# Kernel optimization log

Measured on AMD Instinct MI355X. Metric: run time of the kernel, lower is better.

Reference implementation:

```python
import jax, jax.numpy as jnp
import numpy as np

DEPTH = 10
NUM_FEATURES = 512
NUM_LEAVES = 2 ** DEPTH
TEMPERATURE = 0.1
BATCH = 32768


def _leaf_codes():
    # codes[leaf, i] = bit i (MSB first) of leaf index
    leaves = np.arange(NUM_LEAVES)
    shifts = DEPTH - 1 - np.arange(DEPTH)
    codes = (leaves[:, None] >> shifts[None, :]) & 1
    return jnp.asarray(codes, dtype=jnp.float32)  # [num_leaves, depth]


def setup_inputs() -> dict:
    key = jax.random.key(0)
    k1, k2, k3 = jax.random.split(key, 3)
    x = jax.random.normal(k1, (BATCH, NUM_FEATURES), dtype=jnp.float32)
    feature_weights = jax.random.normal(k2, (DEPTH, NUM_FEATURES), dtype=jnp.float32) * 0.01
    thresholds = jnp.zeros((DEPTH,), dtype=jnp.float32)
    leaf_values = jax.random.normal(k3, (NUM_FEATURES, NUM_LEAVES), dtype=jnp.float32) * 0.01
    return {"x": x, "feature_weights": feature_weights,
            "thresholds": thresholds, "leaf_values": leaf_values}


def reference(x, feature_weights, thresholds, leaf_values):
    codes = _leaf_codes()                                   # [L, D]
    probs = jax.nn.softmax(feature_weights, axis=1)          # [D, F]
    sel = x @ probs.T                                        # [B, D]
    decisions = jax.nn.sigmoid((sel - thresholds) / TEMPERATURE)  # [B, D]
    # leaf_probs[b, l] = prod_d (p*code + (1-p)*(1-code))
    p = decisions[:, None, :]                                # [B, 1, D]
    c = codes[None, :, :]                                    # [1, L, D]
    leaf_probs = jnp.prod(p * c + (1.0 - p) * (1.0 - c), axis=-1)  # [B, L]
    out = leaf_probs @ leaf_values.T                         # [B, F]
    return out
```

## Files before the change

### kernel.cpp

```cpp
#include <hip/hip_runtime.h>
#include <hip/hip_bf16.h>
#include <cstdint>

using u16 = unsigned short;
using u32 = unsigned int;

#define DEPTH 10
#define NF 512
#define NL 1024
#define BATCH_N 32768
#define TEMP_INV 10.0f
#define GBM 128
#define GBN 256
#define GBK 64
#define NSTEP (NL / GBK)

typedef float f32x4 __attribute__((ext_vector_type(4)));
typedef short s16x8 __attribute__((ext_vector_type(8)));
typedef __bf16 bf16x8 __attribute__((ext_vector_type(8)));

__device__ __forceinline__ u16 f2bf(float f) {
  u32 u = __float_as_uint(f);
  u = (u + 0x7fffu + ((u >> 16) & 1u)) >> 16;
  return (u16)u;
}

__device__ __forceinline__ void gld_lds16(const void* g, void* lds) {
  __builtin_amdgcn_global_load_lds(
      (const __attribute__((address_space(1))) void*)g,
      (__attribute__((address_space(3))) void*)lds, 16, 0, 0);
}

__global__ void k_cvt(const float* __restrict__ lv, u16* __restrict__ lvb) {
  int i = (blockIdx.x * blockDim.x + threadIdx.x) * 8;
  float4 a = *(const float4*)(lv + i);
  float4 b = *(const float4*)(lv + i + 4);
  uint4 u;
  u.x = f2bf(a.x) | ((u32)f2bf(a.y) << 16);
  u.y = f2bf(a.z) | ((u32)f2bf(a.w) << 16);
  u.z = f2bf(b.x) | ((u32)f2bf(b.y) << 16);
  u.w = f2bf(b.z) | ((u32)f2bf(b.w) << 16);
  *(uint4*)(lvb + i) = u;
}

__global__ __launch_bounds__(256, 4) void k_sel(const float* __restrict__ x,
                                                const float* __restrict__ fw,
                                                const float* __restrict__ thr,
                                                float* __restrict__ pout) {
  __shared__ float Ps[DEPTH * NF];
  const int tid = threadIdx.x;
  const int lane = tid & 63;
  const int w = tid >> 6;

  for (int d = w; d < DEPTH; d += 4) {
    const float* row = fw + d * NF;
    float v[8];
    float mx = -1e30f;
#pragma unroll
    for (int i = 0; i < 8; ++i) { v[i] = row[lane * 8 + i]; mx = fmaxf(mx, v[i]); }
#pragma unroll
    for (int s = 32; s >= 1; s >>= 1) mx = fmaxf(mx, __shfl_xor(mx, s));
    float sum = 0.f;
#pragma unroll
    for (int i = 0; i < 8; ++i) { v[i] = __expf(v[i] - mx); sum += v[i]; }
#pragma unroll
    for (int s = 32; s >= 1; s >>= 1) sum += __shfl_xor(sum, s);
    float inv = 1.0f / sum;
#pragma unroll
    for (int i = 0; i < 8; ++i) Ps[d * NF + lane * 8 + i] = v[i] * inv;
  }
  __syncthreads();

  const int g = lane & 15;
  const int qr = lane >> 4;
  const int r0 = blockIdx.x * 32 + (w * 4 + qr) * 2;
  const float* xp0 = x + (size_t)r0 * NF + g * 4;
  const float* xp1 = xp0 + NF;

  float a0[DEPTH], a1[DEPTH];
#pragma unroll
  for (int d = 0; d < DEPTH; ++d) { a0[d] = 0.f; a1[d] = 0.f; }
#pragma unroll 2
  for (int i = 0; i < 8; ++i) {
    float4 xv0 = *(const float4*)(xp0 + i * 64);
    float4 xv1 = *(const float4*)(xp1 + i * 64);
    const float* pb = &Ps[i * 64 + g * 4];
#pragma unroll
    for (int d = 0; d < DEPTH; ++d) {
      f32x4 pv = *(const f32x4*)(pb + d * NF);
      a0[d] += xv0.x * pv[0] + xv0.y * pv[1] + xv0.z * pv[2] + xv0.w * pv[3];
      a1[d] += xv1.x * pv[0] + xv1.y * pv[1] + xv1.z * pv[2] + xv1.w * pv[3];
    }
  }
#pragma unroll
  for (int d = 0; d < DEPTH; ++d) {
    a0[d] += __shfl_xor(a0[d], 1); a0[d] += __shfl_xor(a0[d], 2);
    a0[d] += __shfl_xor(a0[d], 4); a0[d] += __shfl_xor(a0[d], 8);
    a1[d] += __shfl_xor(a1[d], 1); a1[d] += __shfl_xor(a1[d], 2);
    a1[d] += __shfl_xor(a1[d], 4); a1[d] += __shfl_xor(a1[d], 8);
  }
  if (g < DEPTH) {
    float s0 = (g == 0) ? a0[0] : (g == 1) ? a0[1] : (g == 2) ? a0[2]
             : (g == 3) ? a0[3] : (g == 4) ? a0[4] : (g == 5) ? a0[5]
             : (g == 6) ? a0[6] : (g == 7) ? a0[7] : (g == 8) ? a0[8] : a0[9];
    float s1 = (g == 0) ? a1[0] : (g == 1) ? a1[1] : (g == 2) ? a1[2]
             : (g == 3) ? a1[3] : (g == 4) ? a1[4] : (g == 5) ? a1[5]
             : (g == 6) ? a1[6] : (g == 7) ? a1[7] : (g == 8) ? a1[8] : a1[9];
    float t = thr[g];
    pout[(size_t)r0 * DEPTH + g]       = 1.0f / (1.0f + __expf(-(s0 - t) * TEMP_INV));
    pout[(size_t)(r0 + 1) * DEPTH + g] = 1.0f / (1.0f + __expf(-(s1 - t) * TEMP_INV));
  }
}

__global__ __launch_bounds__(256, 2) void k_gemm(const u16* __restrict__ B,
                                                 const float* __restrict__ p,
                                                 float* __restrict__ C) {
  __shared__ char smem[65536];
  const int tid = threadIdx.x;
  const int lane = tid & 63;
  const int w = tid >> 6;
  const int wm = w >> 1, wn = w & 1;
  const int bm = blockIdx.x >> 1, bn = blockIdx.x & 1;
  const int brow = bm * GBM, bcol = bn * GBN;
  const int rA = lane & 15, sg = lane >> 4;

  float T[4][8];
  float base0[4], r0_[4], r1_[4], r2_[4], r3_[4], r4_[4];
#pragma unroll
  for (int m = 0; m < 4; ++m) {
    const float* pr = p + (size_t)(brow + wm * 64 + m * 16 + rA) * DEPTH;
    float p0 = pr[0], p1 = pr[1], p2 = pr[2], p3 = pr[3], p4 = pr[4];
    float p5 = pr[5], p6 = pr[6], p7 = pr[7], p8 = pr[8], p9 = pr[9];
    float q0 = 1.f - p0, q1 = 1.f - p1, q2 = 1.f - p2, q3 = 1.f - p3, q4 = 1.f - p4;
    base0[m] = q0 * q1 * q2 * q3 * q4;
    r0_[m] = p0 / q0; r1_[m] = p1 / q1; r2_[m] = p2 / q2;
    r3_[m] = p3 / q3; r4_[m] = p4 / q4;
    float s56 = ((sg & 2) ? p5 : 1.f - p5) * ((sg & 1) ? p6 : 1.f - p6);
    float a7 = 1.f - p7, b7 = p7, a8 = 1.f - p8, b8 = p8, a9 = 1.f - p9, b9 = p9;
#pragma unroll
    for (int j = 0; j < 8; ++j)
      T[m][j] = s56 * ((j & 4) ? b7 : a7) * ((j & 2) ? b8 : a8) * ((j & 1) ? b9 : a9);
  }

  f32x4 acc[4][8];
#pragma unroll
  for (int m = 0; m < 4; ++m)
#pragma unroll
    for (int n = 0; n < 8; ++n) acc[m][n] = {0.f, 0.f, 0.f, 0.f};

  auto STAGE = [&](int step, int buf) {
    char* bsb = smem + buf * 32768;
#pragma unroll
    for (int it = 0; it < 8; ++it) {
      int lin = it * 256 + tid;
      int r = lin >> 3;
      int sl = (lin & 7) ^ (r & 7);
      gld_lds16(B + (size_t)(bcol + r) * NL + step * GBK + sl * 8, bsb + lin * 16);
    }
  };

  STAGE(0, 0);
  asm volatile("s_waitcnt vmcnt(0)" ::: "memory");
  __builtin_amdgcn_s_barrier();

#pragma unroll 1
  for (int kk = 0; kk < NSTEP; ++kk) {
    if (kk < NSTEP - 1) STAGE(kk + 1, (kk + 1) & 1);
    const char* bb = smem + (kk & 1) * 32768;

    float H[4];
#pragma unroll
    for (int m = 0; m < 4; ++m) {
      float g = base0[m] * ((kk & 8) ? r0_[m] : 1.0f);
      g *= (kk & 4) ? r1_[m] : 1.0f;
      g *= (kk & 2) ? r2_[m] : 1.0f;
      g *= (kk & 1) ? r3_[m] : 1.0f;
      H[m] = g;
    }
    {
      bf16x8 af[4];
#pragma unroll
      for (int m = 0; m < 4; ++m)
#pragma unroll
        for (int j = 0; j < 8; ++j) af[m][j] = (__bf16)(H[m] * T[m][j]);
#pragma unroll
      for (int n = 0; n < 8; ++n) {
        int row = wn * 128 + n * 16 + rA;
        bf16x8 bf = __builtin_bit_cast(bf16x8,
            *(const s16x8*)(bb + row * 128 + ((sg ^ (row & 7)) << 4)));
        acc[0][n] = __builtin_amdgcn_mfma_f32_16x16x32_bf16(af[0], bf, acc[0][n], 0, 0, 0);
        acc[1][n] = __builtin_amdgcn_mfma_f32_16x16x32_bf16(af[1], bf, acc[1][n], 0, 0, 0);
        acc[2][n] = __builtin_amdgcn_mfma_f32_16x16x32_bf16(af[2], bf, acc[2][n], 0, 0, 0);
        acc[3][n] = __builtin_amdgcn_mfma_f32_16x16x32_bf16(af[3], bf, acc[3][n], 0, 0, 0);
      }
    }
    {
      bf16x8 af[4];
#pragma unroll
      for (int m = 0; m < 4; ++m) {
        float h1 = H[m] * r4_[m];
#pragma unroll
        for (int j = 0; j < 8; ++j) af[m][j] = (__bf16)(h1 * T[m][j]);
      }
#pragma unroll
      for (int n = 0; n < 8; ++n) {
        int row = wn * 128 + n * 16 + rA;
        bf16x8 bf = __builtin_bit_cast(bf16x8,
            *(const s16x8*)(bb + row * 128 + (((4 + sg) ^ (row & 7)) << 4)));
        acc[0][n] = __builtin_amdgcn_mfma_f32_16x16x32_bf16(af[0], bf, acc[0][n], 0, 0, 0);
        acc[1][n] = __builtin_amdgcn_mfma_f32_16x16x32_bf16(af[1], bf, acc[1][n], 0, 0, 0);
        acc[2][n] = __builtin_amdgcn_mfma_f32_16x16x32_bf16(af[2], bf, acc[2][n], 0, 0, 0);
        acc[3][n] = __builtin_amdgcn_mfma_f32_16x16x32_bf16(af[3], bf, acc[3][n], 0, 0, 0);
      }
    }
    if (kk < NSTEP - 1) {
      asm volatile("s_waitcnt vmcnt(0) lgkmcnt(0)" ::: "memory");
      __builtin_amdgcn_s_barrier();
    }
  }

  const int c0 = lane & 15;
  const int rr = (lane >> 4) * 4;
#pragma unroll
  for (int m = 0; m < 4; ++m)
#pragma unroll
    for (int n = 0; n < 8; ++n) {
      int col = bcol + wn * 128 + n * 16 + c0;
#pragma unroll
      for (int r = 0; r < 4; ++r)
        C[(size_t)(brow + wm * 64 + m * 16 + rr + r) * NF + col] = acc[m][n][r];
    }
}

extern "C" void kernel_launch(void* const* d_in, const int* in_sizes, int n_in,
                              void* d_out, int out_size, void* d_ws, size_t ws_size,
                              hipStream_t stream) {
  const float* x  = (const float*)d_in[0];
  const float* fw = (const float*)d_in[1];
  const float* th = (const float*)d_in[2];
  const float* lv = (const float*)d_in[3];
  float* out = (float*)d_out;

  u16* lvb = (u16*)d_ws;
  float* pbuf = (float*)((char*)d_ws + NF * NL * 2);

  k_cvt<<<(NF * NL / 8) / 256, 256, 0, stream>>>(lv, lvb);
  k_sel<<<BATCH_N / 32, 256, 0, stream>>>(x, fw, th, pbuf);
  k_gemm<<<(BATCH_N / GBM) * 2, 256, 0, stream>>>(lvb, pbuf, out);
}
```

Before: 67.23 us.

## Restructure GEMM into 8-wave blocks with triple-buffered half-K LDS pipeline

Raises the GEMM block from 4 to 8 waves, so each wave owns 32 rows instead of 64 and holds half the accumulators. B tiles are split into 128-column by 64-K halves in a 6-slot LDS ring. Loads are issued two steps ahead in small chunks interleaved with four MFMA phases per K step, and s_setprio is raised around the MFMA bursts. The goal is to overlap global-to-LDS traffic with matrix work and raise per-CU wave parallelism. In exchange it uses 96KB of LDS per block and many more barriers, which may limit residency to one block per CU.

```diff
diff --git a/kernel.cpp b/kernel.cpp
--- a/kernel.cpp
+++ b/kernel.cpp
@@ -13,7 +13,7 @@
 #define GBM 128
 #define GBN 256
 #define GBK 64
-#define NSTEP (NL / GBK)
+#define NSTEP 16
 
 typedef float f32x4 __attribute__((ext_vector_type(4)));
 typedef short s16x8 __attribute__((ext_vector_type(8)));
@@ -112,29 +112,28 @@
   }
 }
 
-__global__ __launch_bounds__(256, 2) void k_gemm(const u16* __restrict__ B,
+__global__ __launch_bounds__(512, 2) void k_gemm(const u16* __restrict__ B,
                                                  const float* __restrict__ p,
                                                  float* __restrict__ C) {
-  __shared__ char smem[65536];
+  __shared__ char smem[98304];
   const int tid = threadIdx.x;
   const int lane = tid & 63;
   const int w = tid >> 6;
-  const int wm = w >> 1, wn = w & 1;
-  const int bm = blockIdx.x >> 1, bn = blockIdx.x & 1;
+  const int wm = w >> 1;
+  const int wn = w & 1;
+  const int bm = (int)blockIdx.x >> 1, bn = (int)blockIdx.x & 1;
   const int brow = bm * GBM, bcol = bn * GBN;
   const int rA = lane & 15, sg = lane >> 4;
 
-  float T[4][8];
-  float base0[4], r0_[4], r1_[4], r2_[4], r3_[4], r4_[4];
-#pragma unroll
-  for (int m = 0; m < 4; ++m) {
-    const float* pr = p + (size_t)(brow + wm * 64 + m * 16 + rA) * DEPTH;
+  float T[2][8], base0[2], R0[2], R1[2], R2[2], R3[2], R4[2];
+#pragma unroll
+  for (int m = 0; m < 2; ++m) {
+    const float* pr = p + (size_t)(brow + wm * 32 + m * 16 + rA) * DEPTH;
     float p0 = pr[0], p1 = pr[1], p2 = pr[2], p3 = pr[3], p4 = pr[4];
     float p5 = pr[5], p6 = pr[6], p7 = pr[7], p8 = pr[8], p9 = pr[9];
     float q0 = 1.f - p0, q1 = 1.f - p1, q2 = 1.f - p2, q3 = 1.f - p3, q4 = 1.f - p4;
     base0[m] = q0 * q1 * q2 * q3 * q4;
-    r0_[m] = p0 / q0; r1_[m] = p1 / q1; r2_[m] = p2 / q2;
-    r3_[m] = p3 / q3; r4_[m] = p4 / q4;
+    R0[m] = p0 / q0; R1[m] = p1 / q1; R2[m] = p2 / q2; R3[m] = p3 / q3; R4[m] = p4 / q4;
     float s56 = ((sg & 2) ? p5 : 1.f - p5) * ((sg & 1) ? p6 : 1.f - p6);
     float a7 = 1.f - p7, b7 = p7, a8 = 1.f - p8, b8 = p8, a9 = 1.f - p9, b9 = p9;
 #pragma unroll
@@ -142,93 +141,108 @@
       T[m][j] = s56 * ((j & 4) ? b7 : a7) * ((j & 2) ? b8 : a8) * ((j & 1) ? b9 : a9);
   }
 
-  f32x4 acc[4][8];
-#pragma unroll
-  for (int m = 0; m < 4; ++m)
+  f32x4 acc[2][8];
+#pragma unroll
+  for (int m = 0; m < 2; ++m)
 #pragma unroll
     for (int n = 0; n < 8; ++n) acc[m][n] = {0.f, 0.f, 0.f, 0.f};
 
-  auto STAGE = [&](int step, int buf) {
-    char* bsb = smem + buf * 32768;
-#pragma unroll
-    for (int it = 0; it < 8; ++it) {
-      int lin = it * 256 + tid;
-      int r = lin >> 3;
-      int sl = (lin & 7) ^ (r & 7);
-      gld_lds16(B + (size_t)(bcol + r) * NL + step * GBK + sl * 8, bsb + lin * 16);
-    }
+  auto STAGE1 = [&](int h, int buf, int it) {
+    int lin = it * 512 + tid;
+    int r = lin >> 3, s = lin & 7;
+    gld_lds16(B + (size_t)(bcol + (h & 1) * 128 + r) * NL + (h >> 1) * GBK + ((s ^ (r & 7)) * 8),
+              smem + buf * 16384 + lin * 16);
   };
 
-  STAGE(0, 0);
-  asm volatile("s_waitcnt vmcnt(0)" ::: "memory");
+#pragma unroll
+  for (int h = 0; h < 4; ++h) { STAGE1(h, h, 0); STAGE1(h, h, 1); }
+  asm volatile("s_waitcnt vmcnt(4)" ::: "memory");
   __builtin_amdgcn_s_barrier();
+
+  int b0 = 0;
+  bf16x8 af0, af1;
+  float Ha, Hb;
+
+#define DO_PHASE(KH, NH, SIDX, TRAILBAR)                                        \
+  {                                                                             \
+    const char* bb = smem + (b0 + wn) * 16384;                                  \
+    int rr0 = ((NH) * 4 + 0) * 16 + rA;                                         \
+    int rr1 = ((NH) * 4 + 1) * 16 + rA;                                         \
+    int rr2 = ((NH) * 4 + 2) * 16 + rA;                                         \
+    int rr3 = ((NH) * 4 + 3) * 16 + rA;                                         \
+    bf16x8 f0 = __builtin_bit_cast(bf16x8,                                      \
+        *(const s16x8*)(bb + rr0 * 128 + ((((KH)*4 + sg) ^ (rr0 & 7)) << 4)));  \
+    bf16x8 f1 = __builtin_bit_cast(bf16x8,                                      \
+        *(const s16x8*)(bb + rr1 * 128 + ((((KH)*4 + sg) ^ (rr1 & 7)) << 4)));  \
+    bf16x8 f2 = __builtin_bit_cast(bf16x8,                                      \
+        *(const s16x8*)(bb + rr2 * 128 + ((((KH)*4 + sg) ^ (rr2 & 7)) << 4)));  \
+    bf16x8 f3 = __builtin_bit_cast(bf16x8,                                      \
+        *(const s16x8*)(bb + rr3 * 128 + ((((KH)*4 + sg) ^ (rr3 & 7)) << 4)));  \
+    if ((SIDX) == 0) {                         \
+      Ha = base0[0] * ((kk & 8) ? R0[0] : 1.f);                                 \
+      Ha *= (kk & 4) ? R1[0] : 1.f;  Ha *= (kk & 2) ? R2[0] : 1.f;              \
+      Ha *= (kk & 1) ? R3[0] : 1.f;                                             \
+      Hb = base0[1] * ((kk & 8) ? R0[1] : 1.f);                                 \
+      Hb *= (kk & 4) ? R1[1] : 1.f;  Hb *= (kk & 2) ? R2[1] : 1.f;              \
+      Hb *= (kk & 1) ? R3[1] : 1.f;                                             \
+      _Pragma("unroll") for (int j = 0; j < 8; ++j) {                           \
+        af0[j] = (__bf16)(Ha * T[0][j]);  af1[j] = (__bf16)(Hb * T[1][j]);      \
+      }                                                                         \
+    }                                                                           \
+    if ((SIDX) == 2) {                                 \
+      Ha *= R4[0];  Hb *= R4[1];                                                \
+      _Pragma("unroll") for (int j = 0; j < 8; ++j) {                           \
+        af0[j] = (__bf16)(Ha * T[0][j]);  af1[j] = (__bf16)(Hb * T[1][j]);      \
+      }                                                                         \
+    }                                                                           \
+    if (kk < NSTEP - 2) {                        \
+      int sb = b0 + 4 + ((SIDX) >> 1); if (sb >= 6) sb -= 6;                    \
+      STAGE1(2 * kk + 4 + ((SIDX) >> 1), sb, (SIDX) & 1);                       \
+    }                                                                           \
+    __builtin_amdgcn_s_barrier();                                               \
+    asm volatile("s_waitcnt lgkmcnt(0)" ::: "memory");                          \
+    __builtin_amdgcn_sched_barrier(0);                                          \
+    __builtin_amdgcn_s_setprio(1);                                              \
+    acc[0][(NH)*4+0] = __builtin_amdgcn_mfma_f32_16x16x32_bf16(af0, f0, acc[0][(NH)*4+0], 0, 0, 0); \
+    acc[1][(NH)*4+0] = __builtin_amdgcn_mfma_f32_16x16x32_bf16(af1, f0, acc[1][(NH)*4+0], 0, 0, 0); \
+    acc[0][(NH)*4+1] = __builtin_amdgcn_mfma_f32_16x16x32_bf16(af0, f1, acc[0][(NH)*4+1], 0, 0, 0); \
+    acc[1][(NH)*4+1] = __builtin_amdgcn_mfma_f32_16x16x32_bf16(af1, f1, acc[1][(NH)*4+1], 0, 0, 0); \
+    acc[0][(NH)*4+2] = __builtin_amdgcn_mfma_f32_16x16x32_bf16(af0, f2, acc[0][(NH)*4+2], 0, 0, 0); \
+    acc[1][(NH)*4+2] = __builtin_amdgcn_mfma_f32_16x16x32_bf16(af1, f2, acc[1][(NH)*4+2], 0, 0, 0); \
+    acc[0][(NH)*4+3] = __builtin_amdgcn_mfma_f32_16x16x32_bf16(af0, f3, acc[0][(NH)*4+3], 0, 0, 0); \
+    acc[1][(NH)*4+3] = __builtin_amdgcn_mfma_f32_16x16x32_bf16(af1, f3, acc[1][(NH)*4+3], 0, 0, 0); \
+    __builtin_amdgcn_s_setprio(0);                                              \
+    if (TRAILBAR) __builtin_amdgcn_s_barrier();                                 \
+  }
 
 #pragma unroll 1
   for (int kk = 0; kk < NSTEP; ++kk) {
-    if (kk < NSTEP - 1) STAGE(kk + 1, (kk + 1) & 1);
-    const char* bb = smem + (kk & 1) * 32768;
-
-    float H[4];
-#pragma unroll
-    for (int m = 0; m < 4; ++m) {
-      float g = base0[m] * ((kk & 8) ? r0_[m] : 1.0f);
-      g *= (kk & 4) ? r1_[m] : 1.0f;
-      g *= (kk & 2) ? r2_[m] : 1.0f;
-      g *= (kk & 1) ? r3_[m] : 1.0f;
-      H[m] = g;
+    DO_PHASE(0, 0, 0, 1)
+    DO_PHASE(0, 1, 1, 1)
+    DO_PHASE(1, 0, 2, 1)
+    DO_PHASE(1, 1, 3, 0)
+    if (kk < NSTEP - 1) {
+      if (kk == NSTEP - 2) {
+        asm volatile("s_waitcnt vmcnt(0)" ::: "memory");
+      } else {
+        asm volatile("s_waitcnt vmcnt(4)" ::: "memory");
+      }
+      __builtin_amdgcn_s_barrier();
+      b0 += 2; if (b0 >= 6) b0 -= 6;
     }
-    {
-      bf16x8 af[4];
-#pragma unroll
-      for (int m = 0; m < 4; ++m)
-#pragma unroll
-        for (int j = 0; j < 8; ++j) af[m][j] = (__bf16)(H[m] * T[m][j]);
-#pragma unroll
-      for (int n = 0; n < 8; ++n) {
-        int row = wn * 128 + n * 16 + rA;
-        bf16x8 bf = __builtin_bit_cast(bf16x8,
-            *(const s16x8*)(bb + row * 128 + ((sg ^ (row & 7)) << 4)));
-        acc[0][n] = __builtin_amdgcn_mfma_f32_16x16x32_bf16(af[0], bf, acc[0][n], 0, 0, 0);
-        acc[1][n] = __builtin_amdgcn_mfma_f32_16x16x32_bf16(af[1], bf, acc[1][n], 0, 0, 0);
-        acc[2][n] = __builtin_amdgcn_mfma_f32_16x16x32_bf16(af[2], bf, acc[2][n], 0, 0, 0);
-        acc[3][n] = __builtin_amdgcn_mfma_f32_16x16x32_bf16(af[3], bf, acc[3][n], 0, 0, 0);
-      }
-    }
-    {
-      bf16x8 af[4];
-#pragma unroll
-      for (int m = 0; m < 4; ++m) {
-        float h1 = H[m] * r4_[m];
-#pragma unroll
-        for (int j = 0; j < 8; ++j) af[m][j] = (__bf16)(h1 * T[m][j]);
-      }
-#pragma unroll
-      for (int n = 0; n < 8; ++n) {
-        int row = wn * 128 + n * 16 + rA;
-        bf16x8 bf = __builtin_bit_cast(bf16x8,
-            *(const s16x8*)(bb + row * 128 + (((4 + sg) ^ (row & 7)) << 4)));
-        acc[0][n] = __builtin_amdgcn_mfma_f32_16x16x32_bf16(af[0], bf, acc[0][n], 0, 0, 0);
-        acc[1][n] = __builtin_amdgcn_mfma_f32_16x16x32_bf16(af[1], bf, acc[1][n], 0, 0, 0);
-        acc[2][n] = __builtin_amdgcn_mfma_f32_16x16x32_bf16(af[2], bf, acc[2][n], 0, 0, 0);
-        acc[3][n] = __builtin_amdgcn_mfma_f32_16x16x32_bf16(af[3], bf, acc[3][n], 0, 0, 0);
-      }
-    }
-    if (kk < NSTEP - 1) {
-      asm volatile("s_waitcnt vmcnt(0) lgkmcnt(0)" ::: "memory");
-      __builtin_amdgcn_s_barrier();
-    }
-  }
+  }
+#undef DO_PHASE
 
   const int c0 = lane & 15;
   const int rr = (lane >> 4) * 4;
 #pragma unroll
-  for (int m = 0; m < 4; ++m)
+  for (int m = 0; m < 2; ++m)
 #pragma unroll
     for (int n = 0; n < 8; ++n) {
       int col = bcol + wn * 128 + n * 16 + c0;
 #pragma unroll
       for (int r = 0; r < 4; ++r)
-        C[(size_t)(brow + wm * 64 + m * 16 + rr + r) * NF + col] = acc[m][n][r];
+        C[(size_t)(brow + wm * 32 + m * 16 + rr + r) * NF + col] = acc[m][n][r];
     }
 }
 
@@ -246,5 +260,5 @@
 
   k_cvt<<<(NF * NL / 8) / 256, 256, 0, stream>>>(lv, lvb);
   k_sel<<<BATCH_N / 32, 256, 0, stream>>>(x, fw, th, pbuf);
-  k_gemm<<<(BATCH_N / GBM) * 2, 256, 0, stream>>>(lvb, pbuf, out);
-}
+  k_gemm<<<(BATCH_N / GBM) * 2, 512, 0, stream>>>(lvb, pbuf, out);
+}
```

New measurement: 76.16 us. +13.3%, slower.

## Use 512-thread GEMM blocks and register-staged LDS loads instead of direct global-to-LDS

Applied to the files above, without the earlier changes.

The GEMM block grows from 4 to 8 waves, so each wave now owns 32 rows instead of 64, halving its accumulator registers and raising the occupancy target. The direct global_load_lds staging is replaced with ordinary global loads into registers, written to the swizzled LDS buffer after the MFMAs, with __syncthreads in place of hand-written waitcnt and barrier. The aim is better latency hiding through more resident waves. In exchange each B fragment read from LDS now feeds only two MFMAs instead of four, and the staging adds VGPR traffic and an extra LDS write pass.

```diff
diff --git a/kernel.cpp b/kernel.cpp
--- a/kernel.cpp
+++ b/kernel.cpp
@@ -13,7 +13,7 @@
 #define GBM 128
 #define GBN 256
 #define GBK 64
-#define NSTEP (NL / GBK)
+#define NSTEP 16
 
 typedef float f32x4 __attribute__((ext_vector_type(4)));
 typedef short s16x8 __attribute__((ext_vector_type(8)));
@@ -23,12 +23,6 @@
   u32 u = __float_as_uint(f);
   u = (u + 0x7fffu + ((u >> 16) & 1u)) >> 16;
   return (u16)u;
-}
-
-__device__ __forceinline__ void gld_lds16(const void* g, void* lds) {
-  __builtin_amdgcn_global_load_lds(
-      (const __attribute__((address_space(1))) void*)g,
-      (__attribute__((address_space(3))) void*)lds, 16, 0, 0);
 }
 
 __global__ void k_cvt(const float* __restrict__ lv, u16* __restrict__ lvb) {
@@ -112,29 +106,28 @@
   }
 }
 
-__global__ __launch_bounds__(256, 2) void k_gemm(const u16* __restrict__ B,
+__global__ __launch_bounds__(512, 4) void k_gemm(const u16* __restrict__ B,
                                                  const float* __restrict__ p,
                                                  float* __restrict__ C) {
   __shared__ char smem[65536];
   const int tid = threadIdx.x;
   const int lane = tid & 63;
   const int w = tid >> 6;
-  const int wm = w >> 1, wn = w & 1;
-  const int bm = blockIdx.x >> 1, bn = blockIdx.x & 1;
+  const int wm = w >> 1;
+  const int wn = w & 1;
+  const int bm = (int)blockIdx.x >> 1, bn = (int)blockIdx.x & 1;
   const int brow = bm * GBM, bcol = bn * GBN;
   const int rA = lane & 15, sg = lane >> 4;
 
-  float T[4][8];
-  float base0[4], r0_[4], r1_[4], r2_[4], r3_[4], r4_[4];
-#pragma unroll
-  for (int m = 0; m < 4; ++m) {
-    const float* pr = p + (size_t)(brow + wm * 64 + m * 16 + rA) * DEPTH;
+  float T[2][8], base0[2], R0[2], R1[2], R2[2], R3[2], R4[2];
+#pragma unroll
+  for (int m = 0; m < 2; ++m) {
+    const float* pr = p + (size_t)(brow + wm * 32 + m * 16 + rA) * DEPTH;
     float p0 = pr[0], p1 = pr[1], p2 = pr[2], p3 = pr[3], p4 = pr[4];
     float p5 = pr[5], p6 = pr[6], p7 = pr[7], p8 = pr[8], p9 = pr[9];
     float q0 = 1.f - p0, q1 = 1.f - p1, q2 = 1.f - p2, q3 = 1.f - p3, q4 = 1.f - p4;
     base0[m] = q0 * q1 * q2 * q3 * q4;
-    r0_[m] = p0 / q0; r1_[m] = p1 / q1; r2_[m] = p2 / q2;
-    r3_[m] = p3 / q3; r4_[m] = p4 / q4;
+    R0[m] = p0 / q0; R1[m] = p1 / q1; R2[m] = p2 / q2; R3[m] = p3 / q3; R4[m] = p4 / q4;
     float s56 = ((sg & 2) ? p5 : 1.f - p5) * ((sg & 1) ? p6 : 1.f - p6);
     float a7 = 1.f - p7, b7 = p7, a8 = 1.f - p8, b8 = p8, a9 = 1.f - p9, b9 = p9;
 #pragma unroll
@@ -142,93 +135,82 @@
       T[m][j] = s56 * ((j & 4) ? b7 : a7) * ((j & 2) ? b8 : a8) * ((j & 1) ? b9 : a9);
   }
 
-  f32x4 acc[4][8];
-#pragma unroll
-  for (int m = 0; m < 4; ++m)
+  f32x4 acc[2][8];
+#pragma unroll
+  for (int m = 0; m < 2; ++m)
 #pragma unroll
     for (int n = 0; n < 8; ++n) acc[m][n] = {0.f, 0.f, 0.f, 0.f};
 
-  auto STAGE = [&](int step, int buf) {
-    char* bsb = smem + buf * 32768;
-#pragma unroll
-    for (int it = 0; it < 8; ++it) {
-      int lin = it * 256 + tid;
-      int r = lin >> 3;
-      int sl = (lin & 7) ^ (r & 7);
-      gld_lds16(B + (size_t)(bcol + r) * NL + step * GBK + sl * 8, bsb + lin * 16);
+  const int sr = tid >> 3;
+  const int ss = tid & 7;
+  const int swz = (ss ^ (sr & 7)) * 16;
+
+  uint4 stg[4];
+  auto STAGE_LOAD = [&](int step) {
+#pragma unroll
+    for (int it = 0; it < 4; ++it) {
+      int r = it * 64 + sr;
+      stg[it] = *(const uint4*)(B + (size_t)(bcol + r) * NL + step * GBK + ss * 8);
     }
   };
-
-  STAGE(0, 0);
-  asm volatile("s_waitcnt vmcnt(0)" ::: "memory");
-  __builtin_amdgcn_s_barrier();
+  auto STAGE_WRITE = [&](int buf) {
+#pragma unroll
+    for (int it = 0; it < 4; ++it) {
+      int r = it * 64 + sr;
+      *(uint4*)(smem + buf * 32768 + r * 128 + swz) = stg[it];
+    }
+  };
+
+  STAGE_LOAD(0);
+  STAGE_WRITE(0);
+  __syncthreads();
 
 #pragma unroll 1
   for (int kk = 0; kk < NSTEP; ++kk) {
-    if (kk < NSTEP - 1) STAGE(kk + 1, (kk + 1) & 1);
+    if (kk < NSTEP - 1) STAGE_LOAD(kk + 1);
     const char* bb = smem + (kk & 1) * 32768;
 
-    float H[4];
-#pragma unroll
-    for (int m = 0; m < 4; ++m) {
-      float g = base0[m] * ((kk & 8) ? r0_[m] : 1.0f);
-      g *= (kk & 4) ? r1_[m] : 1.0f;
-      g *= (kk & 2) ? r2_[m] : 1.0f;
-      g *= (kk & 1) ? r3_[m] : 1.0f;
-      H[m] = g;
-    }
-    {
-      bf16x8 af[4];
-#pragma unroll
-      for (int m = 0; m < 4; ++m)
-#pragma unroll
-        for (int j = 0; j < 8; ++j) af[m][j] = (__bf16)(H[m] * T[m][j]);
+    float Ha = base0[0] * ((kk & 8) ? R0[0] : 1.f);
+    Ha *= (kk & 4) ? R1[0] : 1.f;
+    Ha *= (kk & 2) ? R2[0] : 1.f;
+    Ha *= (kk & 1) ? R3[0] : 1.f;
+    float Hb = base0[1] * ((kk & 8) ? R0[1] : 1.f);
+    Hb *= (kk & 4) ? R1[1] : 1.f;
+    Hb *= (kk & 2) ? R2[1] : 1.f;
+    Hb *= (kk & 1) ? R3[1] : 1.f;
+
+#pragma unroll
+    for (int kh = 0; kh < 2; ++kh) {
+      if (kh == 1) { Ha *= R4[0]; Hb *= R4[1]; }
+      bf16x8 af0, af1;
+#pragma unroll
+      for (int j = 0; j < 8; ++j) {
+        af0[j] = (__bf16)(Ha * T[0][j]);
+        af1[j] = (__bf16)(Hb * T[1][j]);
+      }
 #pragma unroll
       for (int n = 0; n < 8; ++n) {
         int row = wn * 128 + n * 16 + rA;
         bf16x8 bf = __builtin_bit_cast(bf16x8,
-            *(const s16x8*)(bb + row * 128 + ((sg ^ (row & 7)) << 4)));
-        acc[0][n] = __builtin_amdgcn_mfma_f32_16x16x32_bf16(af[0], bf, acc[0][n], 0, 0, 0);
-        acc[1][n] = __builtin_amdgcn_mfma_f32_16x16x32_bf16(af[1], bf, acc[1][n], 0, 0, 0);
-        acc[2][n] = __builtin_amdgcn_mfma_f32_16x16x32_bf16(af[2], bf, acc[2][n], 0, 0, 0);
-        acc[3][n] = __builtin_amdgcn_mfma_f32_16x16x32_bf16(af[3], bf, acc[3][n], 0, 0, 0);
+            *(const s16x8*)(bb + row * 128 + (((kh * 4 + sg) ^ (row & 7)) << 4)));
+        acc[0][n] = __builtin_amdgcn_mfma_f32_16x16x32_bf16(af0, bf, acc[0][n], 0, 0, 0);
+        acc[1][n] = __builtin_amdgcn_mfma_f32_16x16x32_bf16(af1, bf, acc[1][n], 0, 0, 0);
       }
     }
-    {
-      bf16x8 af[4];
-#pragma unroll
-      for (int m = 0; m < 4; ++m) {
-        float h1 = H[m] * r4_[m];
-#pragma unroll
-        for (int j = 0; j < 8; ++j) af[m][j] = (__bf16)(h1 * T[m][j]);
-      }
-#pragma unroll
-      for (int n = 0; n < 8; ++n) {
-        int row = wn * 128 + n * 16 + rA;
-        bf16x8 bf = __builtin_bit_cast(bf16x8,
-            *(const s16x8*)(bb + row * 128 + (((4 + sg) ^ (row & 7)) << 4)));
-        acc[0][n] = __builtin_amdgcn_mfma_f32_16x16x32_bf16(af[0], bf, acc[0][n], 0, 0, 0);
-        acc[1][n] = __builtin_amdgcn_mfma_f32_16x16x32_bf16(af[1], bf, acc[1][n], 0, 0, 0);
-        acc[2][n] = __builtin_amdgcn_mfma_f32_16x16x32_bf16(af[2], bf, acc[2][n], 0, 0, 0);
-        acc[3][n] = __builtin_amdgcn_mfma_f32_16x16x32_bf16(af[3], bf, acc[3][n], 0, 0, 0);
-      }
-    }
-    if (kk < NSTEP - 1) {
-      asm volatile("s_waitcnt vmcnt(0) lgkmcnt(0)" ::: "memory");
-      __builtin_amdgcn_s_barrier();
-    }
+    if (kk < NSTEP - 1) STAGE_WRITE((kk + 1) & 1);
+    __syncthreads();
   }
 
   const int c0 = lane & 15;
   const int rr = (lane >> 4) * 4;
 #pragma unroll
-  for (int m = 0; m < 4; ++m)
+  for (int m = 0; m < 2; ++m)
 #pragma unroll
     for (int n = 0; n < 8; ++n) {
       int col = bcol + wn * 128 + n * 16 + c0;
 #pragma unroll
       for (int r = 0; r < 4; ++r)
-        C[(size_t)(brow + wm * 64 + m * 16 + rr + r) * NF + col] = acc[m][n][r];
+        C[(size_t)(brow + wm * 32 + m * 16 + rr + r) * NF + col] = acc[m][n][r];
     }
 }
 
@@ -246,5 +228,5 @@
 
   k_cvt<<<(NF * NL / 8) / 256, 256, 0, stream>>>(lv, lvb);
   k_sel<<<BATCH_N / 32, 256, 0, stream>>>(x, fw, th, pbuf);
-  k_gemm<<<(BATCH_N / GBM) * 2, 256, 0, stream>>>(lvb, pbuf, out);
-}
+  k_gemm<<<(BATCH_N / GBM) * 2, 512, 0, stream>>>(lvb, pbuf, out);
+}
```

Result: slower. 104.9 us (+56.1%).
